# Performance work log

Hardware: AMD Instinct MI355X
Metric: run time of the kernel (lower is better)

The kernel has to match this reference:

```python
import jax, jax.numpy as jnp
import numpy as np

B, T, I, H = 64, 512, 256, 1024


def setup_inputs() -> dict:
    key = jax.random.key(0)
    ks = jax.random.split(key, 20)
    stdv = float(1.0 / np.sqrt(H))
    u = lambda k, shape: jax.random.uniform(k, shape, jnp.float32, -stdv, stdv)
    d = {
        "inputs": jax.random.normal(ks[0], (B, T, I), jnp.float32),
        "h0": jax.random.normal(ks[1], (1, B, H), jnp.float32),
        "c0": jax.random.normal(ks[2], (1, B, H), jnp.float32),
    }
    names = ["w_ii", "w_hi", "b_ii", "b_hi",
             "w_if", "w_hf", "b_if", "b_hf",
             "w_io", "w_ho", "b_io", "b_ho",
             "w_ig", "w_hg", "b_ig", "b_hg"]
    shapes = {"w_i": (H, I), "w_h": (H, H), "b_i": (H,), "b_h": (H,)}
    for j, n in enumerate(names):
        d[n] = u(ks[3 + j], shapes[n[:3]])
    return d


def reference(inputs, h0, c0,
              w_ii, w_hi, b_ii, b_hi,
              w_if, w_hf, b_if, b_hf,
              w_io, w_ho, b_io, b_ho,
              w_ig, w_hg, b_ig, b_hg):
    # Fuse the 4 gate GEMMs into one: gate order i, f, g, o.
    Wx = jnp.concatenate([w_ii, w_if, w_ig, w_io], axis=0)  # (4H, I)
    Wh = jnp.concatenate([w_hi, w_hf, w_hg, w_ho], axis=0)  # (4H, H)
    b = jnp.concatenate([b_ii + b_hi, b_if + b_hf, b_ig + b_hg, b_io + b_ho], axis=0)  # (4H,)
    # Precompute all input projections in one big GEMM: (T, B, 4H)
    x_proj = jnp.einsum('bti,gi->tbg', inputs, Wx) + b

    def step(carry, xp):
        h, c = carry                       # (B, H), (B, H)
        z = xp + h @ Wh.T                  # (B, 4H)
        i = jax.nn.sigmoid(z[:, :H])
        f = jax.nn.sigmoid(z[:, H:2 * H])
        g = jnp.tanh(z[:, 2 * H:3 * H])
        o = jax.nn.sigmoid(z[:, 3 * H:])
        c = f * c + i * g
        h = o * jnp.tanh(c)
        return (h, c), h

    (h, c), hs = jax.lax.scan(step, (h0[0], c0[0]), x_proj)
    hidden_seq = jnp.transpose(hs, (1, 0, 2))  # (B, T, H)
    return hidden_seq, (h[None], c[None])
```

## Files before the change

### kernel.cpp

```cpp
#include <hip/hip_runtime.h>
#include <hip/hip_bf16.h>

#define TT 512
#define BB 64
#define II 256
#define HH 1024
#define NWG 256
#define MB 32
#define NR 32
#define KTOT 1280
#define ROWB 2048
#define NFLAG 1024

typedef __bf16 bf16x8 __attribute__((ext_vector_type(8)));
typedef float f32x4 __attribute__((ext_vector_type(4)));
typedef unsigned uint32x4 __attribute__((ext_vector_type(4)));
typedef unsigned uint32x2 __attribute__((ext_vector_type(2)));

__device__ inline uint32x4 ld16_sc1(const void* p) {
  uint32x4 r;
  asm volatile("global_load_dwordx4 %0, %1, off sc1" : "=&v"(r) : "v"(p));
  return r;
}


__global__ __launch_bounds__(256) void k_cast_inputs(const float* __restrict__ in,
                                                     __hip_bfloat16* __restrict__ outp) {
  int i = (blockIdx.x * 256 + threadIdx.x) * 4;
  float4 v = *reinterpret_cast<const float4*>(in + i);
  outp[i + 0] = __float2bfloat16(v.x);
  outp[i + 1] = __float2bfloat16(v.y);
  outp[i + 2] = __float2bfloat16(v.z);
  outp[i + 3] = __float2bfloat16(v.w);
}

__global__ __launch_bounds__(256) void k_pack_w(
    const float* __restrict__ wxi, const float* __restrict__ whi,
    const float* __restrict__ wxf, const float* __restrict__ whf,
    const float* __restrict__ wxg, const float* __restrict__ whg,
    const float* __restrict__ wxo, const float* __restrict__ who,
    __hip_bfloat16* __restrict__ Wp) {
  int t = blockIdx.x * 256 + threadIdx.x;
  int p = t / 320;
  int k4 = (t - p * 320) * 4;
  int j = p >> 2, gate = p & 3;
  const float* wx = (gate == 0) ? wxi : (gate == 1) ? wxf : (gate == 2) ? wxg : wxo;
  const float* wh = (gate == 0) ? whi : (gate == 1) ? whf : (gate == 2) ? whg : who;
  float4 v;
  if (k4 < II) v = *reinterpret_cast<const float4*>(wx + (size_t)j * II + k4);
  else         v = *reinterpret_cast<const float4*>(wh + (size_t)j * HH + (k4 - II));
  __hip_bfloat16* o = Wp + (size_t)p * KTOT + k4;
  o[0] = __float2bfloat16(v.x);
  o[1] = __float2bfloat16(v.y);
  o[2] = __float2bfloat16(v.z);
  o[3] = __float2bfloat16(v.w);
}

__global__ __launch_bounds__(256) void k_pack_bias_h0(
    const float* __restrict__ bii, const float* __restrict__ bhi,
    const float* __restrict__ bif, const float* __restrict__ bhf,
    const float* __restrict__ bg,  const float* __restrict__ bhg,
    const float* __restrict__ bio, const float* __restrict__ bho,
    const float* __restrict__ h0, float* __restrict__ biasp,
    __hip_bfloat16* __restrict__ hb, unsigned* __restrict__ flags) {
  int i = blockIdx.x * 256 + threadIdx.x;
  if (i < 4096) {
    int j = i >> 2, gate = i & 3;
    const float* bi = (gate == 0) ? bii : (gate == 1) ? bif : (gate == 2) ? bg : bio;
    const float* bh = (gate == 0) ? bhi : (gate == 1) ? bhf : (gate == 2) ? bhg : bho;
    biasp[i] = bi[j] + bh[j];
  }
  if (i < NFLAG) flags[i] = 0;
  hb[i] = __float2bfloat16(h0[i]);
}


__global__ __launch_bounds__(256, 1) void k_lstm(
    const __hip_bfloat16* __restrict__ xb,
    const __hip_bfloat16* __restrict__ Wp,
    const float* __restrict__ biasp,
    const float* __restrict__ c0,
    __hip_bfloat16* __restrict__ hbuf,
    unsigned* __restrict__ flags,
    float* __restrict__ out)
{
  extern __shared__ __align__(16) char smem[];
  char* Wl = smem;
  char* Hs = smem + 65536;
  char* Zx = smem + 131072;
  char* Ho = smem + 136192;

  const int tid = threadIdx.x;
  const int lane = tid & 63;
  const int wq = tid >> 6;
  const int bt = blockIdx.x >> 7;
  const int gt = blockIdx.x & 127;
  const int b0 = bt * MB;
  const int r0 = gt * NR;

  const int mh = wq >> 1;
  const int nh = wq & 1;
  const int l15 = lane & 15;
  const int kqu = lane >> 4;

  {
    uint32x4 tmp[16];
#pragma unroll
    for (int q = 0; q < 16; ++q) {
      int row = q * 2 + (tid >> 7);
      int u = tid & 127;
      tmp[q] = *reinterpret_cast<const uint32x4*>(Wp + (size_t)(r0 + row) * KTOT + II + u * 8);
    }
#pragma unroll
    for (int q = 0; q < 16; ++q) {
      int row = q * 2 + (tid >> 7);
      int u = tid & 127;
      *reinterpret_cast<uint32x4*>(Wl + row * ROWB + ((u ^ (row & 7)) << 4)) = tmp[q];
    }
  }

  bf16x8 wxr[8];
  {
    const __hip_bfloat16* wsrc = Wp + (size_t)(r0 + nh * 16 + l15) * KTOT + kqu * 8;
#pragma unroll
    for (int kk = 0; kk < 8; ++kk)
      wxr[kk] = *reinterpret_cast<const bf16x8*>(wsrc + kk * 32);
  }

  const int m_e = 4 * kqu + (lane & 3);
  const int tq = (lane >> 2) & 3;
  const int j_l = nh * 4 + tq;
  const int b_l = mh * 16 + m_e;
  const int j_g = gt * 8 + j_l;
  const int b_g = b0 + b_l;
  const float4 bias = *reinterpret_cast<const float4*>(biasp + j_g * 4);
  float c_reg = c0[(size_t)b_g * HH + j_g];

  const int am_row = mh * 16 + l15, am_swz = am_row & 7;
  const int bn_row = nh * 16 + l15, bn_swz = bn_row & 7;
  char* ZxW = Zx + wq * 1280;
  char* HoW = Ho + wq * 128;

  {
    uint32x4 tmp[16];
#pragma unroll
    for (int q = 0; q < 16; ++q) {
      int idx = q * 64 + lane;
      int rl = wq * 8 + (idx >> 7);
      int u = idx & 127;
      tmp[q] = ld16_sc1(hbuf + (size_t)(b0 + rl) * HH + u * 8);
    }
    asm volatile("s_waitcnt vmcnt(0)" ::: "memory");
    __builtin_amdgcn_sched_barrier(0);
#pragma unroll
    for (int q = 0; q < 16; ++q) {
      int idx = q * 64 + lane;
      int rl = wq * 8 + (idx >> 7);
      int u = idx & 127;
      *reinterpret_cast<uint32x4*>(Hs + rl * ROWB + ((u ^ (rl & 7)) << 4)) = tmp[q];
    }
  }

  const __hip_bfloat16* xrowA = xb + (size_t)(b0 + mh * 16 + l15) * (TT * II) + kqu * 8;
  f32x4 accs[4];
#pragma unroll
  for (int q = 0; q < 4; ++q) accs[q] = (f32x4){0.f, 0.f, 0.f, 0.f};
#pragma unroll
  for (int kk = 0; kk < 8; ++kk) {
    bf16x8 xa = *reinterpret_cast<const bf16x8*>(xrowA + kk * 32);
    accs[kk & 3] = __builtin_amdgcn_mfma_f32_16x16x32_bf16(xa, wxr[kk], accs[kk & 3], 0, 0, 0);
  }

  __syncthreads();

  for (int t = 0; t < TT; ++t) {
#pragma unroll
    for (int kk = 0; kk < 32; ++kk) {
      int u = kk * 4 + kqu;
      bf16x8 a = *reinterpret_cast<const bf16x8*>(Hs + am_row * ROWB + ((u ^ am_swz) << 4));
      bf16x8 b = *reinterpret_cast<const bf16x8*>(Wl + bn_row * ROWB + ((u ^ bn_swz) << 4));
      accs[kk & 3] = __builtin_amdgcn_mfma_f32_16x16x32_bf16(a, b, accs[kk & 3], 0, 0, 0);
    }
    f32x4 acc = (accs[0] + accs[1]) + (accs[2] + accs[3]);

    *reinterpret_cast<f32x4*>(ZxW + l15 * 80 + kqu * 16) = acc;
    asm volatile("s_waitcnt lgkmcnt(0)" ::: "memory");
    __builtin_amdgcn_sched_barrier(0);
    float zi = *reinterpret_cast<const float*>(ZxW + (4 * tq + 0) * 80 + m_e * 4) + bias.x;
    float zf = *reinterpret_cast<const float*>(ZxW + (4 * tq + 1) * 80 + m_e * 4) + bias.y;
    float zg = *reinterpret_cast<const float*>(ZxW + (4 * tq + 2) * 80 + m_e * 4) + bias.z;
    float zo = *reinterpret_cast<const float*>(ZxW + (4 * tq + 3) * 80 + m_e * 4) + bias.w;

    float ig = 1.f / (1.f + __expf(-zi));
    float fg = 1.f / (1.f + __expf(-zf));
    float gg = 2.f / (1.f + __expf(-2.f * zg)) - 1.f;
    float og = 1.f / (1.f + __expf(-zo));
    c_reg = fg * c_reg + ig * gg;
    float tc = 2.f / (1.f + __expf(-2.f * c_reg)) - 1.f;
    float h = og * tc;

    if (t == TT - 1) {
      out[(size_t)b_g * (TT * HH) + (size_t)t * HH + j_g] = h;
      out[(size_t)BB * TT * HH + (size_t)b_g * HH + j_g] = h;
      out[(size_t)BB * TT * HH + BB * HH + (size_t)b_g * HH + j_g] = c_reg;
      break;
    }

    __hip_bfloat16 hb16 = __float2bfloat16(h);
    *reinterpret_cast<unsigned short*>(HoW + m_e * 8 + tq * 2) =
        *reinterpret_cast<unsigned short*>(&hb16);
    asm volatile("s_waitcnt lgkmcnt(0)" ::: "memory");
    __builtin_amdgcn_sched_barrier(0);

    const int nxt = (t + 1) & 1;
    if (lane < 16) {
      uint32x2 hv = *reinterpret_cast<const uint32x2*>(HoW + lane * 8);
      __hip_bfloat16* dst = hbuf + (size_t)nxt * (BB * HH)
                          + (size_t)(b0 + mh * 16 + lane) * HH + gt * 8 + nh * 4;
      asm volatile("global_store_dwordx2 %0, %1, off sc1" :: "v"(dst), "v"(hv) : "memory");
    }
    asm volatile("s_waitcnt vmcnt(0)" ::: "memory");
    if (lane == 0) {
      unsigned gen = (unsigned)t + 1u;
      asm volatile("global_store_dword %0, %1, off sc1"
                   :: "v"(flags + bt * 512 + gt * 4 + wq), "v"(gen) : "memory");
    }

    out[(size_t)b_g * (TT * HH) + (size_t)t * HH + j_g] = h;
#pragma unroll
    for (int q = 0; q < 4; ++q) accs[q] = (f32x4){0.f, 0.f, 0.f, 0.f};
    {
      const __hip_bfloat16* xp = xrowA + (size_t)(t + 1) * II;
#pragma unroll
      for (int kk = 0; kk < 8; ++kk) {
        bf16x8 xa = *reinterpret_cast<const bf16x8*>(xp + kk * 32);
        accs[kk & 3] = __builtin_amdgcn_mfma_f32_16x16x32_bf16(xa, wxr[kk], accs[kk & 3], 0, 0, 0);
      }
    }

    {
      const unsigned target = (unsigned)t + 1u;
      const unsigned* fp = flags + bt * 512 + lane * 8;
      uint32x4 f1, f2;
      int ok;
      do {
        asm volatile("global_load_dwordx4 %0, %2, off sc1\n\t"
                     "global_load_dwordx4 %1, %3, off sc1\n\t"
                     "s_waitcnt vmcnt(0)"
                     : "=&v"(f1), "=&v"(f2) : "v"(fp), "v"(fp + 4) : "memory");
        ok = (f1.x >= target) && (f1.y >= target) && (f1.z >= target) && (f1.w >= target)
          && (f2.x >= target) && (f2.y >= target) && (f2.z >= target) && (f2.w >= target);
      } while (!__all(ok));
    }

    {
      uint32x4 tmp[16];
      const __hip_bfloat16* hsrc = hbuf + (size_t)nxt * (BB * HH);
#pragma unroll
      for (int q = 0; q < 16; ++q) {
        int idx = q * 64 + lane;
        int rl = wq * 8 + (idx >> 7);
        int u = idx & 127;
        tmp[q] = ld16_sc1(hsrc + (size_t)(b0 + rl) * HH + u * 8);
      }
      asm volatile("s_waitcnt vmcnt(0)" ::: "memory");
      __builtin_amdgcn_sched_barrier(0);
#pragma unroll
      for (int q = 0; q < 16; ++q) {
        int idx = q * 64 + lane;
        int rl = wq * 8 + (idx >> 7);
        int u = idx & 127;
        *reinterpret_cast<uint32x4*>(Hs + rl * ROWB + ((u ^ (rl & 7)) << 4)) = tmp[q];
      }
    }
    __syncthreads();
  }
}


extern "C" void kernel_launch(void* const* d_in, const int* in_sizes, int n_in,
                              void* d_out, int out_size, void* d_ws, size_t ws_size,
                              hipStream_t stream) {
  (void)in_sizes; (void)n_in; (void)out_size; (void)ws_size;
  const float* inputs = (const float*)d_in[0];
  const float* h0 = (const float*)d_in[1];
  const float* c0 = (const float*)d_in[2];
  const float* w_ii = (const float*)d_in[3];
  const float* w_hi = (const float*)d_in[4];
  const float* b_ii = (const float*)d_in[5];
  const float* b_hi = (const float*)d_in[6];
  const float* w_if = (const float*)d_in[7];
  const float* w_hf = (const float*)d_in[8];
  const float* b_if = (const float*)d_in[9];
  const float* b_hf = (const float*)d_in[10];
  const float* w_io = (const float*)d_in[11];
  const float* w_ho = (const float*)d_in[12];
  const float* b_io = (const float*)d_in[13];
  const float* b_ho = (const float*)d_in[14];
  const float* w_ig = (const float*)d_in[15];
  const float* w_hg = (const float*)d_in[16];
  const float* b_ig = (const float*)d_in[17];
  const float* b_hg = (const float*)d_in[18];

  char* ws = (char*)d_ws;
  __hip_bfloat16* xb    = (__hip_bfloat16*)ws;
  __hip_bfloat16* Wp    = (__hip_bfloat16*)(ws + 16777216);
  float*          biasp = (float*)(ws + 27262976);
  __hip_bfloat16* hbuf  = (__hip_bfloat16*)(ws + 27279360);
  unsigned*       flags = (unsigned*)(ws + 27541504);
  float* out = (float*)d_out;

  k_cast_inputs<<<8192, 256, 0, stream>>>(inputs, xb);
  k_pack_w<<<5120, 256, 0, stream>>>(w_ii, w_hi, w_if, w_hf, w_ig, w_hg, w_io, w_ho, Wp);
  k_pack_bias_h0<<<256, 256, 0, stream>>>(b_ii, b_hi, b_if, b_hf, b_ig, b_hg,
                                          b_io, b_ho, h0, biasp, hbuf, flags);

  const int lds_bytes = 136704;
  hipFuncSetAttribute((const void*)k_lstm,
                      hipFuncAttributeMaxDynamicSharedMemorySize, lds_bytes);
  void* args[] = {(void*)&xb, (void*)&Wp, (void*)&biasp, (void*)&c0,
                  (void*)&hbuf, (void*)&flags, (void*)&out};
  hipLaunchCooperativeKernel((void*)k_lstm, dim3(NWG), dim3(256), args,
                             lds_bytes, stream);
}
```

Measured before the change: 2.316 ms.

## Retile LSTM workgroups to 16 batch rows by 64 gate rows with split LDS/register weights

```diff
diff --git a/kernel.cpp b/kernel.cpp
--- a/kernel.cpp
+++ b/kernel.cpp
@@ -6,10 +6,13 @@
 #define II 256
 #define HH 1024
 #define NWG 256
-#define MB 32
-#define NR 32
+#define MB 16
+#define NJ 16
+#define NR 64
 #define KTOT 1280
-#define ROWB 2048
+#define WU 120
+#define WROWB 1920
+#define HROWB 2048
 #define NFLAG 1024
 
 typedef __bf16 bf16x8 __attribute__((ext_vector_type(8)));
@@ -86,82 +89,94 @@
 {
   extern __shared__ __align__(16) char smem[];
   char* Wl = smem;
-  char* Hs = smem + 65536;
-  char* Zx = smem + 131072;
-  char* Ho = smem + 136192;
+  char* Hs = smem + 122880;
+  char* Zx = smem + 155648;
+  char* Ho = smem + 160768;
 
   const int tid = threadIdx.x;
   const int lane = tid & 63;
   const int wq = tid >> 6;
-  const int bt = blockIdx.x >> 7;
-  const int gt = blockIdx.x & 127;
+  const int bt = blockIdx.x >> 6;
+  const int gt = blockIdx.x & 63;
   const int b0 = bt * MB;
   const int r0 = gt * NR;
 
-  const int mh = wq >> 1;
-  const int nh = wq & 1;
   const int l15 = lane & 15;
   const int kqu = lane >> 4;
 
   {
+    const int u = tid & 127;
+    const bool act = u < WU;
     uint32x4 tmp[16];
 #pragma unroll
     for (int q = 0; q < 16; ++q) {
       int row = q * 2 + (tid >> 7);
-      int u = tid & 127;
-      tmp[q] = *reinterpret_cast<const uint32x4*>(Wp + (size_t)(r0 + row) * KTOT + II + u * 8);
+      if (act) tmp[q] = *reinterpret_cast<const uint32x4*>(
+          Wp + (size_t)(r0 + row) * KTOT + II + u * 8);
     }
 #pragma unroll
     for (int q = 0; q < 16; ++q) {
       int row = q * 2 + (tid >> 7);
-      int u = tid & 127;
-      *reinterpret_cast<uint32x4*>(Wl + row * ROWB + ((u ^ (row & 7)) << 4)) = tmp[q];
-    }
-  }
-
-  bf16x8 wxr[8];
+      if (act) *reinterpret_cast<uint32x4*>(Wl + row * WROWB + ((u ^ (row & 7)) << 4)) = tmp[q];
+    }
+#pragma unroll
+    for (int q = 0; q < 16; ++q) {
+      int row = 32 + q * 2 + (tid >> 7);
+      if (act) tmp[q] = *reinterpret_cast<const uint32x4*>(
+          Wp + (size_t)(r0 + row) * KTOT + II + u * 8);
+    }
+#pragma unroll
+    for (int q = 0; q < 16; ++q) {
+      int row = 32 + q * 2 + (tid >> 7);
+      if (act) *reinterpret_cast<uint32x4*>(Wl + row * WROWB + ((u ^ (row & 7)) << 4)) = tmp[q];
+    }
+  }
+
+  const int brow = r0 + wq * 16 + l15;
+  bf16x8 wxr[8], wht0, wht1;
   {
-    const __hip_bfloat16* wsrc = Wp + (size_t)(r0 + nh * 16 + l15) * KTOT + kqu * 8;
+    const __hip_bfloat16* ws = Wp + (size_t)brow * KTOT + kqu * 8;
 #pragma unroll
     for (int kk = 0; kk < 8; ++kk)
-      wxr[kk] = *reinterpret_cast<const bf16x8*>(wsrc + kk * 32);
+      wxr[kk] = *reinterpret_cast<const bf16x8*>(ws + kk * 32);
+    wht0 = *reinterpret_cast<const bf16x8*>(ws + II + 960);
+    wht1 = *reinterpret_cast<const bf16x8*>(ws + II + 992);
   }
 
   const int m_e = 4 * kqu + (lane & 3);
   const int tq = (lane >> 2) & 3;
-  const int j_l = nh * 4 + tq;
-  const int b_l = mh * 16 + m_e;
-  const int j_g = gt * 8 + j_l;
-  const int b_g = b0 + b_l;
+  const int j_g = gt * NJ + wq * 4 + tq;
+  const int b_g = b0 + m_e;
   const float4 bias = *reinterpret_cast<const float4*>(biasp + j_g * 4);
   float c_reg = c0[(size_t)b_g * HH + j_g];
 
-  const int am_row = mh * 16 + l15, am_swz = am_row & 7;
-  const int bn_row = nh * 16 + l15, bn_swz = bn_row & 7;
+  const int hs_swz = l15 & 7;
+  const int bn_row = wq * 16 + l15;
+  const int bn_swz = bn_row & 7;
   char* ZxW = Zx + wq * 1280;
   char* HoW = Ho + wq * 128;
 
   {
-    uint32x4 tmp[16];
-#pragma unroll
-    for (int q = 0; q < 16; ++q) {
+    uint32x4 tmp[8];
+#pragma unroll
+    for (int q = 0; q < 8; ++q) {
       int idx = q * 64 + lane;
-      int rl = wq * 8 + (idx >> 7);
+      int rl = wq * 4 + (idx >> 7);
       int u = idx & 127;
       tmp[q] = ld16_sc1(hbuf + (size_t)(b0 + rl) * HH + u * 8);
     }
     asm volatile("s_waitcnt vmcnt(0)" ::: "memory");
     __builtin_amdgcn_sched_barrier(0);
 #pragma unroll
-    for (int q = 0; q < 16; ++q) {
+    for (int q = 0; q < 8; ++q) {
       int idx = q * 64 + lane;
-      int rl = wq * 8 + (idx >> 7);
+      int rl = wq * 4 + (idx >> 7);
       int u = idx & 127;
-      *reinterpret_cast<uint32x4*>(Hs + rl * ROWB + ((u ^ (rl & 7)) << 4)) = tmp[q];
-    }
-  }
-
-  const __hip_bfloat16* xrowA = xb + (size_t)(b0 + mh * 16 + l15) * (TT * II) + kqu * 8;
+      *reinterpret_cast<uint32x4*>(Hs + rl * HROWB + ((u ^ (rl & 7)) << 4)) = tmp[q];
+    }
+  }
+
+  const __hip_bfloat16* xrowA = xb + (size_t)(b0 + l15) * (TT * II) + kqu * 8;
   f32x4 accs[4];
 #pragma unroll
   for (int q = 0; q < 4; ++q) accs[q] = (f32x4){0.f, 0.f, 0.f, 0.f};
@@ -175,11 +190,21 @@
 
   for (int t = 0; t < TT; ++t) {
 #pragma unroll
-    for (int kk = 0; kk < 32; ++kk) {
+    for (int kk = 0; kk < 30; ++kk) {
       int u = kk * 4 + kqu;
-      bf16x8 a = *reinterpret_cast<const bf16x8*>(Hs + am_row * ROWB + ((u ^ am_swz) << 4));
-      bf16x8 b = *reinterpret_cast<const bf16x8*>(Wl + bn_row * ROWB + ((u ^ bn_swz) << 4));
+      bf16x8 a = *reinterpret_cast<const bf16x8*>(Hs + l15 * HROWB + ((u ^ hs_swz) << 4));
+      bf16x8 b = *reinterpret_cast<const bf16x8*>(Wl + bn_row * WROWB + ((u ^ bn_swz) << 4));
       accs[kk & 3] = __builtin_amdgcn_mfma_f32_16x16x32_bf16(a, b, accs[kk & 3], 0, 0, 0);
+    }
+    {
+      int u = 120 + kqu;
+      bf16x8 a = *reinterpret_cast<const bf16x8*>(Hs + l15 * HROWB + ((u ^ hs_swz) << 4));
+      accs[2] = __builtin_amdgcn_mfma_f32_16x16x32_bf16(a, wht0, accs[2], 0, 0, 0);
+    }
+    {
+      int u = 124 + kqu;
+      bf16x8 a = *reinterpret_cast<const bf16x8*>(Hs + l15 * HROWB + ((u ^ hs_swz) << 4));
+      accs[3] = __builtin_amdgcn_mfma_f32_16x16x32_bf16(a, wht1, accs[3], 0, 0, 0);
     }
     f32x4 acc = (accs[0] + accs[1]) + (accs[2] + accs[3]);
 
@@ -216,14 +241,14 @@
     if (lane < 16) {
       uint32x2 hv = *reinterpret_cast<const uint32x2*>(HoW + lane * 8);
       __hip_bfloat16* dst = hbuf + (size_t)nxt * (BB * HH)
-                          + (size_t)(b0 + mh * 16 + lane) * HH + gt * 8 + nh * 4;
+                          + (size_t)(b0 + lane) * HH + gt * NJ + wq * 4;
       asm volatile("global_store_dwordx2 %0, %1, off sc1" :: "v"(dst), "v"(hv) : "memory");
     }
     asm volatile("s_waitcnt vmcnt(0)" ::: "memory");
     if (lane == 0) {
       unsigned gen = (unsigned)t + 1u;
       asm volatile("global_store_dword %0, %1, off sc1"
-                   :: "v"(flags + bt * 512 + gt * 4 + wq), "v"(gen) : "memory");
+                   :: "v"(flags + bt * 256 + gt * 4 + wq), "v"(gen) : "memory");
     }
 
     out[(size_t)b_g * (TT * HH) + (size_t)t * HH + j_g] = h;
@@ -240,37 +265,34 @@
 
     {
       const unsigned target = (unsigned)t + 1u;
-      const unsigned* fp = flags + bt * 512 + lane * 8;
-      uint32x4 f1, f2;
+      const unsigned* fp = flags + bt * 256 + lane * 4;
+      uint32x4 f;
       int ok;
       do {
-        asm volatile("global_load_dwordx4 %0, %2, off sc1\n\t"
-                     "global_load_dwordx4 %1, %3, off sc1\n\t"
-                     "s_waitcnt vmcnt(0)"
-                     : "=&v"(f1), "=&v"(f2) : "v"(fp), "v"(fp + 4) : "memory");
-        ok = (f1.x >= target) && (f1.y >= target) && (f1.z >= target) && (f1.w >= target)
-          && (f2.x >= target) && (f2.y >= target) && (f2.z >= target) && (f2.w >= target);
+        asm volatile("global_load_dwordx4 %0, %1, off sc1\n\ts_waitcnt vmcnt(0)"
+                     : "=&v"(f) : "v"(fp) : "memory");
+        ok = (f.x >= target) && (f.y >= target) && (f.z >= target) && (f.w >= target);
       } while (!__all(ok));
     }
 
     {
-      uint32x4 tmp[16];
+      uint32x4 tmp[8];
       const __hip_bfloat16* hsrc = hbuf + (size_t)nxt * (BB * HH);
 #pragma unroll
-      for (int q = 0; q < 16; ++q) {
+      for (int q = 0; q < 8; ++q) {
         int idx = q * 64 + lane;
-        int rl = wq * 8 + (idx >> 7);
+        int rl = wq * 4 + (idx >> 7);
         int u = idx & 127;
         tmp[q] = ld16_sc1(hsrc + (size_t)(b0 + rl) * HH + u * 8);
       }
       asm volatile("s_waitcnt vmcnt(0)" ::: "memory");
       __builtin_amdgcn_sched_barrier(0);
 #pragma unroll
-      for (int q = 0; q < 16; ++q) {
+      for (int q = 0; q < 8; ++q) {
         int idx = q * 64 + lane;
-        int rl = wq * 8 + (idx >> 7);
+        int rl = wq * 4 + (idx >> 7);
         int u = idx & 127;
-        *reinterpret_cast<uint32x4*>(Hs + rl * ROWB + ((u ^ (rl & 7)) << 4)) = tmp[q];
+        *reinterpret_cast<uint32x4*>(Hs + rl * HROWB + ((u ^ (rl & 7)) << 4)) = tmp[q];
       }
     }
     __syncthreads();
@@ -315,7 +337,7 @@
   k_pack_bias_h0<<<256, 256, 0, stream>>>(b_ii, b_hi, b_if, b_hf, b_ig, b_hg,
                                           b_io, b_ho, h0, biasp, hbuf, flags);
 
-  const int lds_bytes = 136704;
+  const int lds_bytes = 161280;
   hipFuncSetAttribute((const void*)k_lstm,
                       hipFuncAttributeMaxDynamicSharedMemorySize, lds_bytes);
   void* args[] = {(void*)&xb, (void*)&Wp, (void*)&biasp, (void*)&c0,
```

After: 2.181 ms. 5.8% less time.
